# Kernel optimization log

Hardware: AMD Instinct MI355X
Metric: run time of the kernel (lower is better)

The kernel has to match this reference:

```python
import jax, jax.numpy as jnp
import numpy as np
import math

B, S, H, D = 2, 2048, 16, 64

def setup_inputs() -> dict:
    key = jax.random.key(0)
    kq, kk, kv, kb, km = jax.random.split(key, 5)
    q = jax.random.normal(kq, (B, S, H, D), dtype=jnp.float32)
    k = jax.random.normal(kk, (B, S, H, D), dtype=jnp.float32)
    v = jax.random.normal(kv, (B, S, H, D), dtype=jnp.float32)
    attn_bias = jax.random.normal(kb, (B, H, S, S), dtype=jnp.float32)
    mask = jax.random.randint(km, (B, S, S), 0, 2) > 0  # bool, True = masked
    return {"q": q, "k": k, "v": v, "attn_bias": attn_bias, "mask": mask}

def reference(q, k, v, attn_bias, mask):
    # [B,S,H,D] -> [B,H,S,D]
    qh = jnp.transpose(q, (0, 2, 1, 3))
    kh = jnp.transpose(k, (0, 2, 1, 3))
    vh = jnp.transpose(v, (0, 2, 1, 3))
    scale = math.sqrt(D)  # NOTE: source MULTIPLIES q by sqrt(head_dim)
    scores = jnp.einsum('bhqd,bhkd->bhqk', qh * scale, kh) + attn_bias
    # source fills masked positions with 0 (not -inf) before softmax
    scores = jnp.where(mask[:, None, :, :], 0.0, scores)
    p = jax.nn.softmax(scores, axis=-1)
    out = jnp.einsum('bhqk,bhkd->bhqd', p, vh)
    return jnp.transpose(out, (0, 2, 1, 3))  # [B,S,H,D]
```

## Files before the change

### kernel.cpp

```cpp
#include <hip/hip_runtime.h>

#define Bq 2
#define Sq 2048
#define Hq 16
#define Dq 64
#define QT 64
#define KT 128
#define NTILE (Sq/KT)

#define GLDS(gsrc, ldst) __builtin_amdgcn_global_load_lds( \
    (const __attribute__((address_space(1))) void*)(gsrc), \
    (__attribute__((address_space(3))) void*)(ldst), 16, 0, 0)

__global__ __launch_bounds__(512, 4)
void attn_fwd(const float* __restrict__ q,
              const float* __restrict__ k,
              const float* __restrict__ v,
              const float* __restrict__ bias,
              const int* __restrict__ mask,
              float* __restrict__ out)
{
  __shared__ float qs[QT*Dq];
  __shared__ float ks[KT*Dq];
  __shared__ float vs[KT*Dq];

  const int tid  = threadIdx.x;
  const int lane = tid & 63;
  const int wv   = tid >> 6;

  const int bid = (int)blockIdx.x;
  const int lid = ((bid & 7) << 7) | (bid >> 3);
  const int qt  = lid & 31;
  const int bh  = lid >> 5;
  const int h   = bh & (Hq - 1);
  const int b   = bh >> 4;
  const int q0  = qt * QT;
  const int qw  = q0 + wv*8;

  const float* qg = q + ((size_t)(b*Sq + q0)*Hq + h)*Dq;
  const float* kg = k + ((size_t)b*Sq*Hq + h)*Dq;
  const float* vg = v + ((size_t)b*Sq*Hq + h)*Dq;
  const float* bw = bias + ((size_t)((b*Hq + h)*Sq + qw))*Sq;
  const int*   mw = mask + ((size_t)(b*Sq + qw))*Sq;

  #pragma unroll
  for (int r = 0; r < 2; ++r) {
    const int fo  = r*2048 + tid*4;
    const int row = fo >> 6, col = fo & 63;
    float4 t4 = *(const float4*)(qg + (size_t)row*(Hq*Dq) + col);
    t4.x *= 8.f; t4.y *= 8.f; t4.z *= 8.f; t4.w *= 8.f;
    *(float4*)(&qs[fo]) = t4;
  }

  float o[8][8];
  float m[8], l[8], s0[8], s1[8];
  #pragma unroll
  for (int qi = 0; qi < 8; ++qi) {
    m[qi] = -3.0e38f; l[qi] = 0.f;
    #pragma unroll
    for (int dd = 0; dd < 8; ++dd) o[qi][dd] = 0.f;
  }

  const int swf = (lane & 7) << 2;
  const int g   = lane >> 3, c = lane & 7;
  const int vo0 = (c*8)     ^ (g << 2);
  const int vo1 = (c*8 + 4) ^ (g << 2);
  float* pw = &ks[wv*1024];

  for (int tt = 0; tt < NTILE; ++tt) {
    const int j0 = tt*KT;

    __syncthreads();

    #pragma unroll
    for (int r = 0; r < 4; ++r) {
      const int fo  = r*2048 + tid*4;
      const int row = fo >> 6;
      const int col = (fo & 63) ^ ((row & 7) << 2);
      GLDS(kg + (size_t)(j0 + row)*(Hq*Dq) + col, &ks[r*2048 + wv*256]);
      GLDS(vg + (size_t)(j0 + row)*(Hq*Dq) + col, &vs[r*2048 + wv*256]);
    }

    const float* bb = bw + j0 + lane;
    const int*   mm = mw + j0 + lane;
    unsigned mb = 0;
    #pragma unroll
    for (int qi = 0; qi < 8; ++qi) {
      s0[qi] = bb[(size_t)qi*Sq];
      s1[qi] = bb[(size_t)qi*Sq + 64];
      if (mm[(size_t)qi*Sq])      mb |= 1u << (2*qi);
      if (mm[(size_t)qi*Sq + 64]) mb |= 2u << (2*qi);
    }

    __syncthreads();

    const float* kr0  = &ks[lane*64];
    const float* kr1  = &ks[(lane+64)*64];
    const float* qrow = &qs[wv*512];
    #pragma unroll 2
    for (int t = 0; t < 16; ++t) {
      const int off = (t*4) ^ swf;
      const float4 ka = *(const float4*)(kr0 + off);
      const float4 kb = *(const float4*)(kr1 + off);
      #pragma unroll
      for (int qi = 0; qi < 8; ++qi) {
        const float4 qv = *(const float4*)(qrow + qi*64 + t*4);
        s0[qi] = fmaf(qv.x, ka.x, s0[qi]);
        s0[qi] = fmaf(qv.y, ka.y, s0[qi]);
        s0[qi] = fmaf(qv.z, ka.z, s0[qi]);
        s0[qi] = fmaf(qv.w, ka.w, s0[qi]);
        s1[qi] = fmaf(qv.x, kb.x, s1[qi]);
        s1[qi] = fmaf(qv.y, kb.y, s1[qi]);
        s1[qi] = fmaf(qv.z, kb.z, s1[qi]);
        s1[qi] = fmaf(qv.w, kb.w, s1[qi]);
      }
    }

    #pragma unroll
    for (int qi = 0; qi < 8; ++qi) {
      if (mb & (1u << (2*qi))) s0[qi] = 0.f;
      if (mb & (2u << (2*qi))) s1[qi] = 0.f;
    }

    #pragma unroll
    for (int qi = 0; qi < 8; ++qi) {
      float tm = fmaxf(s0[qi], s1[qi]);
      #pragma unroll
      for (int off = 32; off; off >>= 1) tm = fmaxf(tm, __shfl_xor(tm, off, 64));
      const float mn = fmaxf(m[qi], tm);
      const float sc = __expf(m[qi] - mn);
      const float p0 = __expf(s0[qi] - mn);
      const float p1 = __expf(s1[qi] - mn);
      float ls = p0 + p1;
      #pragma unroll
      for (int off = 32; off; off >>= 1) ls += __shfl_xor(ls, off, 64);
      l[qi] = l[qi]*sc + ls;
      m[qi] = mn;
      s0[qi] = p0; s1[qi] = p1;
      #pragma unroll
      for (int dd = 0; dd < 8; ++dd) o[qi][dd] *= sc;
    }

    __syncthreads();

    #pragma unroll
    for (int qi = 0; qi < 8; ++qi) {
      pw[qi*128 + lane]      = s0[qi];
      pw[qi*128 + lane + 64] = s1[qi];
    }

    #pragma unroll 2
    for (int jj = 0; jj < 16; ++jj) {
      const int j = jj*8 + g;
      const float4 va = *(const float4*)(&vs[j*64 + vo0]);
      const float4 vb = *(const float4*)(&vs[j*64 + vo1]);
      #pragma unroll
      for (int qi = 0; qi < 8; ++qi) {
        const float p = pw[qi*128 + j];
        o[qi][0] = fmaf(p, va.x, o[qi][0]);
        o[qi][1] = fmaf(p, va.y, o[qi][1]);
        o[qi][2] = fmaf(p, va.z, o[qi][2]);
        o[qi][3] = fmaf(p, va.w, o[qi][3]);
        o[qi][4] = fmaf(p, vb.x, o[qi][4]);
        o[qi][5] = fmaf(p, vb.y, o[qi][5]);
        o[qi][6] = fmaf(p, vb.z, o[qi][6]);
        o[qi][7] = fmaf(p, vb.w, o[qi][7]);
      }
    }
  }

  #pragma unroll
  for (int qi = 0; qi < 8; ++qi) {
    #pragma unroll
    for (int dd = 0; dd < 8; ++dd) {
      float t = o[qi][dd];
      t += __shfl_xor(t, 8, 64);
      t += __shfl_xor(t, 16, 64);
      t += __shfl_xor(t, 32, 64);
      o[qi][dd] = t;
    }
  }

  float og[8]; float lg = l[0];
  #pragma unroll
  for (int dd = 0; dd < 8; ++dd) og[dd] = o[0][dd];
  #pragma unroll
  for (int qi = 1; qi < 8; ++qi) {
    const bool sel = (g == qi);
    lg = sel ? l[qi] : lg;
    #pragma unroll
    for (int dd = 0; dd < 8; ++dd) og[dd] = sel ? o[qi][dd] : og[dd];
  }
  const float rl = 1.0f / lg;

  float* op = out + ((size_t)(b*Sq + qw + g)*Hq + h)*Dq + c*8;
  float4 oa, ob;
  oa.x = og[0]*rl; oa.y = og[1]*rl; oa.z = og[2]*rl; oa.w = og[3]*rl;
  ob.x = og[4]*rl; ob.y = og[5]*rl; ob.z = og[6]*rl; ob.w = og[7]*rl;
  *(float4*)op       = oa;
  *(float4*)(op + 4) = ob;
}

extern "C" void kernel_launch(void* const* d_in, const int* in_sizes, int n_in,
                              void* d_out, int out_size, void* d_ws, size_t ws_size,
                              hipStream_t stream)
{
  const float* q    = (const float*)d_in[0];
  const float* k    = (const float*)d_in[1];
  const float* v    = (const float*)d_in[2];
  const float* bias = (const float*)d_in[3];
  const int*   mask = (const int*)d_in[4];
  float*       out  = (float*)d_out;

  dim3 grid(Bq*Hq*(Sq/QT));
  attn_fwd<<<grid, dim3(512), 0, stream>>>(q, k, v, bias, mask, out);
}
```

Measured before the change: 1.455 ms.

## Permute P layout for float2 reads, skip unchanged-max rescale, set waves_per_eu

Stores softmax probabilities in LDS in a permuted order so each lane reads two consecutive P values with one float2 load in the PV loop, halving P LDS reads per FMA. The online-softmax rescale of o and l is skipped when the running max did not change. The occupancy hint switches from min-blocks launch bounds to amdgpu_waves_per_eu(4,4). The rescale branch is wave-uniform, but the permuted stores may cause LDS bank conflicts, and the occupancy attribute changes the register budget.

```diff
diff --git a/kernel.cpp b/kernel.cpp
--- a/kernel.cpp
+++ b/kernel.cpp
@@ -12,7 +12,7 @@
     (const __attribute__((address_space(1))) void*)(gsrc), \
     (__attribute__((address_space(3))) void*)(ldst), 16, 0, 0)
 
-__global__ __launch_bounds__(512, 4)
+__global__ __launch_bounds__(512) __attribute__((amdgpu_waves_per_eu(4, 4)))
 void attn_fwd(const float* __restrict__ q,
               const float* __restrict__ k,
               const float* __restrict__ v,
@@ -61,10 +61,11 @@
     for (int dd = 0; dd < 8; ++dd) o[qi][dd] = 0.f;
   }
 
-  const int swf = (lane & 7) << 2;
-  const int g   = lane >> 3, c = lane & 7;
-  const int vo0 = (c*8)     ^ (g << 2);
-  const int vo1 = (c*8 + 4) ^ (g << 2);
+  const int swf  = (lane & 7) << 2;
+  const int g    = lane >> 3, c = lane & 7;
+  const int vo0  = (c*8)     ^ (g << 2);
+  const int vo1  = (c*8 + 4) ^ (g << 2);
+  const int pidx = (lane & 7)*16 + (lane >> 3);
   float* pw = &ks[wv*1024];
 
   for (int tt = 0; tt < NTILE; ++tt) {
@@ -128,43 +129,58 @@
       #pragma unroll
       for (int off = 32; off; off >>= 1) tm = fmaxf(tm, __shfl_xor(tm, off, 64));
       const float mn = fmaxf(m[qi], tm);
-      const float sc = __expf(m[qi] - mn);
       const float p0 = __expf(s0[qi] - mn);
       const float p1 = __expf(s1[qi] - mn);
       float ls = p0 + p1;
       #pragma unroll
       for (int off = 32; off; off >>= 1) ls += __shfl_xor(ls, off, 64);
-      l[qi] = l[qi]*sc + ls;
-      m[qi] = mn;
+      if (mn != m[qi]) {
+        const float sc = __expf(m[qi] - mn);
+        l[qi] = l[qi]*sc + ls;
+        m[qi] = mn;
+        #pragma unroll
+        for (int dd = 0; dd < 8; ++dd) o[qi][dd] *= sc;
+      } else {
+        l[qi] += ls;
+      }
       s0[qi] = p0; s1[qi] = p1;
-      #pragma unroll
-      for (int dd = 0; dd < 8; ++dd) o[qi][dd] *= sc;
     }
 
     __syncthreads();
 
     #pragma unroll
     for (int qi = 0; qi < 8; ++qi) {
-      pw[qi*128 + lane]      = s0[qi];
-      pw[qi*128 + lane + 64] = s1[qi];
+      pw[qi*128 + pidx]     = s0[qi];
+      pw[qi*128 + pidx + 8] = s1[qi];
     }
 
     #pragma unroll 2
-    for (int jj = 0; jj < 16; ++jj) {
-      const int j = jj*8 + g;
-      const float4 va = *(const float4*)(&vs[j*64 + vo0]);
-      const float4 vb = *(const float4*)(&vs[j*64 + vo1]);
+    for (int jj = 0; jj < 8; ++jj) {
+      const int ja = jj*16 + g;
+      const int jb = ja + 8;
+      const float4 va0 = *(const float4*)(&vs[ja*64 + vo0]);
+      const float4 va1 = *(const float4*)(&vs[ja*64 + vo1]);
+      const float4 vb0 = *(const float4*)(&vs[jb*64 + vo0]);
+      const float4 vb1 = *(const float4*)(&vs[jb*64 + vo1]);
       #pragma unroll
       for (int qi = 0; qi < 8; ++qi) {
-        const float p = pw[qi*128 + j];
-        o[qi][0] = fmaf(p, va.x, o[qi][0]);
-        o[qi][1] = fmaf(p, va.y, o[qi][1]);
-        o[qi][2] = fmaf(p, va.z, o[qi][2]);
-        o[qi][3] = fmaf(p, va.w, o[qi][3]);
-        o[qi][4] = fmaf(p, vb.x, o[qi][4]);
-        o[qi][5] = fmaf(p, vb.y, o[qi][5]);
-        o[qi][6] = fmaf(p, vb.z, o[qi][6]);
-        o[qi][7] = fmaf(p, vb.w, o[qi][7]);
+        const float2 pp = *(const float2*)(&pw[qi*128 + g*16 + jj*2]);
+        o[qi][0] = fmaf(pp.x, va0.x, o[qi][0]);
+        o[qi][1] = fmaf(pp.x, va0.y, o[qi][1]);
+        o[qi][2] = fmaf(pp.x, va0.z, o[qi][2]);
+        o[qi][3] = fmaf(pp.x, va0.w, o[qi][3]);
+        o[qi][4] = fmaf(pp.x, va1.x, o[qi][4]);
+        o[qi][5] = fmaf(pp.x, va1.y, o[qi][5]);
+        o[qi][6] = fmaf(pp.x, va1.z, o[qi][6]);
+        o[qi][7] = fmaf(pp.x, va1.w, o[qi][7]);
+        o[qi][0] = fmaf(pp.y, vb0.x, o[qi][0]);
+        o[qi][1] = fmaf(pp.y, vb0.y, o[qi][1]);
+        o[qi][2] = fmaf(pp.y, vb0.z, o[qi][2]);
+        o[qi][3] = fmaf(pp.y, vb0.w, o[qi][3]);
+        o[qi][4] = fmaf(pp.y, vb1.x, o[qi][4]);
+        o[qi][5] = fmaf(pp.y, vb1.y, o[qi][5]);
+        o[qi][6] = fmaf(pp.y, vb1.z, o[qi][6]);
+        o[qi][7] = fmaf(pp.y, vb1.w, o[qi][7]);
       }
     }
   }
```

Result: slower. 1.559 ms (+7.1%).

## Remap PV lane tiling to 4 dims by 4 keys with vectorized P reads

Applied to the files above, without the earlier changes.

Changes the P·V loop so each lane owns 4 output dims and 4 consecutive key rows, not 8 dims and 1 key row. P values are read as float4 from LDS and the V reads match the swizzled layout. This halves the output accumulator registers and cuts cross-lane reduction shuffles. It also skips the rescale exp and multiply when the running max does not change, and relaxes the launch bounds to a waves_per_eu range. The branch adds some divergence cost, and the new V access pattern may bring LDS bank conflicts.

```diff
diff --git a/kernel.cpp b/kernel.cpp
--- a/kernel.cpp
+++ b/kernel.cpp
@@ -12,7 +12,7 @@
     (const __attribute__((address_space(1))) void*)(gsrc), \
     (__attribute__((address_space(3))) void*)(ldst), 16, 0, 0)
 
-__global__ __launch_bounds__(512, 4)
+__global__ __launch_bounds__(512) __attribute__((amdgpu_waves_per_eu(2, 4)))
 void attn_fwd(const float* __restrict__ q,
               const float* __restrict__ k,
               const float* __restrict__ v,
@@ -52,19 +52,23 @@
     *(float4*)(&qs[fo]) = t4;
   }
 
-  float o[8][8];
+  float o[8][4];
   float m[8], l[8], s0[8], s1[8];
   #pragma unroll
   for (int qi = 0; qi < 8; ++qi) {
     m[qi] = -3.0e38f; l[qi] = 0.f;
     #pragma unroll
-    for (int dd = 0; dd < 8; ++dd) o[qi][dd] = 0.f;
+    for (int d = 0; d < 4; ++d) o[qi][d] = 0.f;
   }
 
   const int swf = (lane & 7) << 2;
-  const int g   = lane >> 3, c = lane & 7;
-  const int vo0 = (c*8)     ^ (g << 2);
-  const int vo1 = (c*8 + 4) ^ (g << 2);
+  const int g2  = lane >> 4;
+  const int cc  = lane & 15;
+  const int vr0 = g2*4 + 0, vr1 = g2*4 + 1, vr2 = g2*4 + 2, vr3 = g2*4 + 3;
+  const int vof0 = vr0*64 + ((cc*4) ^ ((vr0 & 7) << 2));
+  const int vof1 = vr1*64 + ((cc*4) ^ ((vr1 & 7) << 2));
+  const int vof2 = vr2*64 + ((cc*4) ^ ((vr2 & 7) << 2));
+  const int vof3 = vr3*64 + ((cc*4) ^ ((vr3 & 7) << 2));
   float* pw = &ks[wv*1024];
 
   for (int tt = 0; tt < NTILE; ++tt) {
@@ -128,17 +132,21 @@
       #pragma unroll
       for (int off = 32; off; off >>= 1) tm = fmaxf(tm, __shfl_xor(tm, off, 64));
       const float mn = fmaxf(m[qi], tm);
-      const float sc = __expf(m[qi] - mn);
       const float p0 = __expf(s0[qi] - mn);
       const float p1 = __expf(s1[qi] - mn);
       float ls = p0 + p1;
       #pragma unroll
       for (int off = 32; off; off >>= 1) ls += __shfl_xor(ls, off, 64);
-      l[qi] = l[qi]*sc + ls;
-      m[qi] = mn;
+      if (mn != m[qi]) {
+        const float sc = __expf(m[qi] - mn);
+        l[qi] = l[qi]*sc + ls;
+        m[qi] = mn;
+        #pragma unroll
+        for (int d = 0; d < 4; ++d) o[qi][d] *= sc;
+      } else {
+        l[qi] += ls;
+      }
       s0[qi] = p0; s1[qi] = p1;
-      #pragma unroll
-      for (int dd = 0; dd < 8; ++dd) o[qi][dd] *= sc;
     }
 
     __syncthreads();
@@ -149,22 +157,31 @@
       pw[qi*128 + lane + 64] = s1[qi];
     }
 
-    #pragma unroll 2
-    for (int jj = 0; jj < 16; ++jj) {
-      const int j = jj*8 + g;
-      const float4 va = *(const float4*)(&vs[j*64 + vo0]);
-      const float4 vb = *(const float4*)(&vs[j*64 + vo1]);
+    #pragma unroll
+    for (int jj = 0; jj < 8; ++jj) {
+      const float4 va = *(const float4*)(&vs[jj*1024 + vof0]);
+      const float4 vb = *(const float4*)(&vs[jj*1024 + vof1]);
+      const float4 vc = *(const float4*)(&vs[jj*1024 + vof2]);
+      const float4 vd = *(const float4*)(&vs[jj*1024 + vof3]);
       #pragma unroll
       for (int qi = 0; qi < 8; ++qi) {
-        const float p = pw[qi*128 + j];
-        o[qi][0] = fmaf(p, va.x, o[qi][0]);
-        o[qi][1] = fmaf(p, va.y, o[qi][1]);
-        o[qi][2] = fmaf(p, va.z, o[qi][2]);
-        o[qi][3] = fmaf(p, va.w, o[qi][3]);
-        o[qi][4] = fmaf(p, vb.x, o[qi][4]);
-        o[qi][5] = fmaf(p, vb.y, o[qi][5]);
-        o[qi][6] = fmaf(p, vb.z, o[qi][6]);
-        o[qi][7] = fmaf(p, vb.w, o[qi][7]);
+        const float4 pp = *(const float4*)(&pw[qi*128 + jj*16 + g2*4]);
+        o[qi][0] = fmaf(pp.x, va.x, o[qi][0]);
+        o[qi][1] = fmaf(pp.x, va.y, o[qi][1]);
+        o[qi][2] = fmaf(pp.x, va.z, o[qi][2]);
+        o[qi][3] = fmaf(pp.x, va.w, o[qi][3]);
+        o[qi][0] = fmaf(pp.y, vb.x, o[qi][0]);
+        o[qi][1] = fmaf(pp.y, vb.y, o[qi][1]);
+        o[qi][2] = fmaf(pp.y, vb.z, o[qi][2]);
+        o[qi][3] = fmaf(pp.y, vb.w, o[qi][3]);
+        o[qi][0] = fmaf(pp.z, vc.x, o[qi][0]);
+        o[qi][1] = fmaf(pp.z, vc.y, o[qi][1]);
+        o[qi][2] = fmaf(pp.z, vc.z, o[qi][2]);
+        o[qi][3] = fmaf(pp.z, vc.w, o[qi][3]);
+        o[qi][0] = fmaf(pp.w, vd.x, o[qi][0]);
+        o[qi][1] = fmaf(pp.w, vd.y, o[qi][1]);
+        o[qi][2] = fmaf(pp.w, vd.z, o[qi][2]);
+        o[qi][3] = fmaf(pp.w, vd.w, o[qi][3]);
       }
     }
   }
@@ -172,33 +189,36 @@
   #pragma unroll
   for (int qi = 0; qi < 8; ++qi) {
     #pragma unroll
-    for (int dd = 0; dd < 8; ++dd) {
-      float t = o[qi][dd];
-      t += __shfl_xor(t, 8, 64);
+    for (int d = 0; d < 4; ++d) {
+      float t = o[qi][d];
       t += __shfl_xor(t, 16, 64);
       t += __shfl_xor(t, 32, 64);
-      o[qi][dd] = t;
-    }
-  }
-
-  float og[8]; float lg = l[0];
-  #pragma unroll
-  for (int dd = 0; dd < 8; ++dd) og[dd] = o[0][dd];
-  #pragma unroll
-  for (int qi = 1; qi < 8; ++qi) {
-    const bool sel = (g == qi);
-    lg = sel ? l[qi] : lg;
-    #pragma unroll
-    for (int dd = 0; dd < 8; ++dd) og[dd] = sel ? o[qi][dd] : og[dd];
-  }
-  const float rl = 1.0f / lg;
-
-  float* op = out + ((size_t)(b*Sq + qw + g)*Hq + h)*Dq + c*8;
-  float4 oa, ob;
-  oa.x = og[0]*rl; oa.y = og[1]*rl; oa.z = og[2]*rl; oa.w = og[3]*rl;
-  ob.x = og[4]*rl; ob.y = og[5]*rl; ob.z = og[6]*rl; ob.w = og[7]*rl;
-  *(float4*)op       = oa;
-  *(float4*)(op + 4) = ob;
+      o[qi][d] = t;
+    }
+  }
+
+  float la = l[0], lb = l[4];
+  float oa[4], ob[4];
+  #pragma unroll
+  for (int d = 0; d < 4; ++d) { oa[d] = o[0][d]; ob[d] = o[4][d]; }
+  #pragma unroll
+  for (int s = 1; s < 4; ++s) {
+    const bool sel = (g2 == s);
+    la = sel ? l[s]   : la;
+    lb = sel ? l[s+4] : lb;
+    #pragma unroll
+    for (int d = 0; d < 4; ++d) {
+      oa[d] = sel ? o[s][d]   : oa[d];
+      ob[d] = sel ? o[s+4][d] : ob[d];
+    }
+  }
+  const float ra = 1.0f / la, rb = 1.0f / lb;
+
+  float4 w4;
+  w4.x = oa[0]*ra; w4.y = oa[1]*ra; w4.z = oa[2]*ra; w4.w = oa[3]*ra;
+  *(float4*)(out + ((size_t)(b*Sq + qw + g2)*Hq + h)*Dq + cc*4) = w4;
+  w4.x = ob[0]*rb; w4.y = ob[1]*rb; w4.z = ob[2]*rb; w4.w = ob[3]*rb;
+  *(float4*)(out + ((size_t)(b*Sq + qw + g2 + 4)*Hq + h)*Dq + cc*4) = w4;
 }
 
 extern "C" void kernel_launch(void* const* d_in, const int* in_sizes, int n_in,
```

Result: slower. 1.513 ms (+4.0%).
